# Performance work log

Hardware: AMD Instinct MI355X
Metric: run time of the kernel (lower is better)

Reference implementation:

```python
import jax, jax.numpy as jnp
import numpy as np

N_VOXELS = 400000
GRID = 128
KSIZE = 3
GROUPS = 4
C_IN = 64
C_OUT = 64


def _build_rulebook(n, grid, ksize, seed=0):
    """Build submanifold-conv neighbor map on host with numpy.

    Returns coords-free neighbor_idx [n, ksize**3] int32; entry k is the index of
    the active voxel at offset k from voxel i, or -1 if that site is inactive.
    """
    rng = np.random.default_rng(seed)
    lin = rng.choice(grid ** 3, size=n, replace=False).astype(np.int64)
    x = lin // (grid * grid)
    y = (lin // grid) % grid
    z = lin % grid
    order = np.argsort(lin)
    sorted_keys = lin[order]
    r = ksize // 2
    nb = np.full((n, ksize ** 3), -1, dtype=np.int32)
    k = 0
    for dx in range(-r, r + 1):
        for dy in range(-r, r + 1):
            for dz in range(-r, r + 1):
                nx, ny, nz = x + dx, y + dy, z + dz
                inb = (nx >= 0) & (nx < grid) & (ny >= 0) & (ny < grid) & (nz >= 0) & (nz < grid)
                nkey = nx * grid * grid + ny * grid + nz
                pos = np.searchsorted(sorted_keys, nkey)
                pos_c = np.minimum(pos, n - 1)
                found = inb & (sorted_keys[pos_c] == nkey)
                nb[:, k] = np.where(found, order[pos_c], -1).astype(np.int32)
                k += 1
    return nb


def setup_inputs() -> dict:
    key = jax.random.key(0)
    k1, k2, k3 = jax.random.split(key, 3)
    cpg_in = C_IN // GROUPS
    cpg_out = C_OUT // GROUPS
    features = jax.random.normal(k1, (N_VOXELS, C_IN), dtype=jnp.float32)
    # weight[g, k, ci, co] for each group g and kernel offset k
    weight = jax.random.normal(k2, (GROUPS, KSIZE ** 3, cpg_in, cpg_out), dtype=jnp.float32) * (1.0 / np.sqrt(cpg_in * KSIZE ** 3))
    bias = jax.random.normal(k3, (C_OUT,), dtype=jnp.float32) * 0.01
    neighbor_idx = jnp.asarray(_build_rulebook(N_VOXELS, GRID, KSIZE))
    return {"features": features, "weight": weight, "bias": bias, "neighbor_idx": neighbor_idx}


def reference(features, weight, bias, neighbor_idx):
    # Grouped submanifold sparse conv: gather -> grouped matmul -> accumulate,
    # over the fixed set of K^3 kernel offsets (output sites == input sites).
    N = features.shape[0]
    G, K, cin, cout = weight.shape
    feat = features.reshape(N, G, cin)
    mask = neighbor_idx >= 0                      # [N, K]
    idx = jnp.where(mask, neighbor_idx, 0)        # safe gather index
    out = jnp.zeros((N, G, cout), dtype=features.dtype)
    for k in range(K):  # K=27 fixed small loop over kernel offsets
        gath = feat[idx[:, k]] * mask[:, k, None, None].astype(features.dtype)  # [N, G, cin]
        out = out + jnp.einsum('ngc,gcd->ngd', gath, weight[:, k])
    out = out.reshape(N, G * cout) + bias
    return out
```

## Files before the change

kernel.cpp:

```cpp
#include <hip/hip_runtime.h>
#include <hip/hip_fp16.h>

#define NVOX 400000
#define KVOL 27
#define CTOT 64
#define NTILES (NVOX / 16)
#define NPAIR 14
#define WFRAG_HALVES (4 * NPAIR * 64 * 8)

#define FEATH_OFF 0
#define WFRAG_OFF 51200000

typedef __attribute__((ext_vector_type(8))) _Float16 half8;
typedef __attribute__((ext_vector_type(4))) float float4v;

__global__ void cvt_feat_kernel(const float* __restrict__ f, _Float16* __restrict__ fh) {
    int t = blockIdx.x * blockDim.x + threadIdx.x;
    const int total = NVOX * CTOT / 8;
    if (t >= total) return;
    const float4* fp = (const float4*)f + (size_t)t * 2;
    float4 a = fp[0], b = fp[1];
    union { _Float16 h[8]; uint4 u; } r;
    r.h[0] = (_Float16)a.x; r.h[1] = (_Float16)a.y;
    r.h[2] = (_Float16)a.z; r.h[3] = (_Float16)a.w;
    r.h[4] = (_Float16)b.x; r.h[5] = (_Float16)b.y;
    r.h[6] = (_Float16)b.z; r.h[7] = (_Float16)b.w;
    ((uint4*)fh)[t] = r.u;
}

__global__ void cvt_w_kernel(const float* __restrict__ w, _Float16* __restrict__ wf) {
    int t = blockIdx.x * blockDim.x + threadIdx.x;
    if (t >= WFRAG_HALVES) return;
    int j = t & 7;
    int l = (t >> 3) & 63;
    int gp = t >> 9;
    int p = gp % NPAIR;
    int g = gp / NPAIR;
    int co = l & 15;
    int quad = l >> 4;
    int ko = 2 * p + (quad >> 1);
    int ci = (quad & 1) * 8 + j;
    float val = (ko < KVOL) ? w[((g * KVOL + ko) * 16 + ci) * 16 + co] : 0.f;
    wf[t] = (_Float16)val;
}

__global__ __launch_bounds__(256) void conv_main_kernel(
        const _Float16* __restrict__ fh,
        const uint4*    __restrict__ wfrag,
        const float*    __restrict__ bias,
        const int*      __restrict__ nb,
        float* __restrict__ out) {
    __shared__ int s_nb[16 * 28];
    const int tile = blockIdx.x;
    const int t = threadIdx.x;

    const int* src = nb + (size_t)tile * (16 * KVOL);
    for (int j = t; j < 16 * KVOL; j += 256) {
        int v = j / KVOL;
        int k = j - v * KVOL;
        s_nb[v * 28 + k] = src[j];
    }
    if (t < 16) s_nb[t * 28 + 27] = -1;

    const int lane = t & 63;
    const int g = t >> 6;
    const int v = lane & 15;
    const int quad = lane >> 4;
    const int q2 = quad >> 1;
    const int half = quad & 1;

    uint4 wB[NPAIR];
#pragma unroll
    for (int p = 0; p < NPAIR; ++p)
        wB[p] = wfrag[(g * NPAIR + p) * 64 + lane];

    __syncthreads();

    int idx[NPAIR];
#pragma unroll
    for (int p = 0; p < NPAIR; ++p)
        idx[p] = s_nb[v * 28 + 2 * p + q2];

    const _Float16* fbase = fh + g * 16 + half * 8;
    const _Float16* zp = (const _Float16*)wfrag + 6912;

    uint4 a[NPAIR];
#pragma unroll
    for (int p = 0; p < NPAIR; ++p) {
        const _Float16* rp = (idx[p] >= 0) ? (fbase + (size_t)idx[p] * CTOT) : zp;
        a[p] = *(const uint4*)rp;
    }
    __builtin_amdgcn_sched_barrier(0);

    float4v acc0 = {0.f, 0.f, 0.f, 0.f};
    float4v acc1 = {0.f, 0.f, 0.f, 0.f};
#pragma unroll
    for (int p = 0; p < NPAIR; p += 2) {
        acc0 = __builtin_amdgcn_mfma_f32_16x16x32_f16(
            __builtin_bit_cast(half8, a[p]),
            __builtin_bit_cast(half8, wB[p]), acc0, 0, 0, 0);
        acc1 = __builtin_amdgcn_mfma_f32_16x16x32_f16(
            __builtin_bit_cast(half8, a[p + 1]),
            __builtin_bit_cast(half8, wB[p + 1]), acc1, 0, 0, 0);
    }

    const int co = lane & 15;
    const float breg = bias[g * 16 + co];
    float* ob = out + ((size_t)(tile * 16 + quad * 4)) * CTOT + g * 16 + co;
#pragma unroll
    for (int r = 0; r < 4; ++r)
        ob[(size_t)r * CTOT] = acc0[r] + acc1[r] + breg;
}

extern "C" void kernel_launch(void* const* d_in, const int* in_sizes, int n_in,
                              void* d_out, int out_size, void* d_ws, size_t ws_size,
                              hipStream_t stream) {
    const float* features = (const float*)d_in[0];
    const float* weight   = (const float*)d_in[1];
    const float* bias     = (const float*)d_in[2];
    const int*   nb       = (const int*)d_in[3];
    float* out = (float*)d_out;

    char* ws = (char*)d_ws;
    _Float16* featH = (_Float16*)(ws + FEATH_OFF);
    _Float16* wf    = (_Float16*)(ws + WFRAG_OFF);

    cvt_feat_kernel<<<(NVOX * CTOT / 8 + 255) / 256, 256, 0, stream>>>(features, featH);
    cvt_w_kernel<<<(WFRAG_HALVES + 255) / 256, 256, 0, stream>>>(weight, wf);
    conv_main_kernel<<<NTILES, 256, 0, stream>>>(featH, (const uint4*)wf, bias, nb, out);
}
```

Before: 330.4 us.

## Process multiple tiles per block with double-buffered neighbor staging and XCD remap

Each workgroup now handles 10 consecutive 16-voxel tiles, so weight fragments are loaded once per block rather than once per tile. The neighbor-index staging is double-buffered in shared memory, and the gather for the next tile is issued before the MFMAs of the current one to overlap memory latency with compute. Block IDs are remapped so that contiguous tile ranges land on the same XCD for cache locality, and inactive neighbors are zeroed with a predicate instead of a load from a zero pointer. This raises register pressure through two fragment arrays, and there is one barrier per tile.

```diff
diff --git a/kernel.cpp b/kernel.cpp
--- a/kernel.cpp
+++ b/kernel.cpp
@@ -6,6 +6,8 @@
 #define CTOT 64
 #define NTILES (NVOX / 16)
 #define NPAIR 14
+#define TPB 10
+#define NBLOCKS (NTILES / TPB)
 #define WFRAG_HALVES (4 * NPAIR * 64 * 8)
 
 #define FEATH_OFF 0
@@ -44,72 +46,102 @@
     wf[t] = (_Float16)val;
 }
 
-__global__ __launch_bounds__(256) void conv_main_kernel(
+__global__ __launch_bounds__(256, 2) void conv_main_kernel(
         const _Float16* __restrict__ fh,
         const uint4*    __restrict__ wfrag,
         const float*    __restrict__ bias,
         const int*      __restrict__ nb,
         float* __restrict__ out) {
-    __shared__ int s_nb[16 * 28];
-    const int tile = blockIdx.x;
+    __shared__ int s_nb[2][16 * KVOL];
     const int t = threadIdx.x;
-
-    const int* src = nb + (size_t)tile * (16 * KVOL);
-    for (int j = t; j < 16 * KVOL; j += 256) {
-        int v = j / KVOL;
-        int k = j - v * KVOL;
-        s_nb[v * 28 + k] = src[j];
-    }
-    if (t < 16) s_nb[t * 28 + 27] = -1;
-
     const int lane = t & 63;
     const int g = t >> 6;
     const int v = lane & 15;
     const int quad = lane >> 4;
     const int q2 = quad >> 1;
     const int half = quad & 1;
+    const int co = lane & 15;
+
+    {
+    }
+    const int q_ = NBLOCKS / 8, r_ = NBLOCKS % 8;
+    const int xcd = blockIdx.x % 8;
+    const int chunk = blockIdx.x / 8;
+    const int wgid = (xcd < r_ ? xcd * (q_ + 1) : r_ * (q_ + 1) + (xcd - r_) * q_) + chunk;
+    const int tile0 = wgid * TPB;
 
     uint4 wB[NPAIR];
 #pragma unroll
     for (int p = 0; p < NPAIR; ++p)
         wB[p] = wfrag[(g * NPAIR + p) * 64 + lane];
 
-    __syncthreads();
+    const _Float16* fbase = fh + g * 16 + half * 8;
+    const float breg = bias[g * 16 + co];
+    const int vb = v * KVOL;
 
-    int idx[NPAIR];
-#pragma unroll
-    for (int p = 0; p < NPAIR; ++p)
-        idx[p] = s_nb[v * 28 + 2 * p + q2];
-
-    const _Float16* fbase = fh + g * 16 + half * 8;
-    const _Float16* zp = (const _Float16*)wfrag + 6912;
-
-    uint4 a[NPAIR];
-#pragma unroll
-    for (int p = 0; p < NPAIR; ++p) {
-        const _Float16* rp = (idx[p] >= 0) ? (fbase + (size_t)idx[p] * CTOT) : zp;
-        a[p] = *(const uint4*)rp;
-    }
-    __builtin_amdgcn_sched_barrier(0);
-
-    float4v acc0 = {0.f, 0.f, 0.f, 0.f};
-    float4v acc1 = {0.f, 0.f, 0.f, 0.f};
-#pragma unroll
-    for (int p = 0; p < NPAIR; p += 2) {
-        acc0 = __builtin_amdgcn_mfma_f32_16x16x32_f16(
-            __builtin_bit_cast(half8, a[p]),
-            __builtin_bit_cast(half8, wB[p]), acc0, 0, 0, 0);
-        acc1 = __builtin_amdgcn_mfma_f32_16x16x32_f16(
-            __builtin_bit_cast(half8, a[p + 1]),
-            __builtin_bit_cast(half8, wB[p + 1]), acc1, 0, 0, 0);
+#define STAGE(b, tile)                                              \
+    {                                                               \
+        const int* src = nb + (size_t)(tile) * (16 * KVOL);         \
+        for (int j = t; j < 16 * KVOL; j += 256)                    \
+            s_nb[(b)][j] = src[j];                                  \
     }
 
-    const int co = lane & 15;
-    const float breg = bias[g * 16 + co];
-    float* ob = out + ((size_t)(tile * 16 + quad * 4)) * CTOT + g * 16 + co;
+#define GATHER(dst, b)                                              \
+    {                                                               \
+        int ix[NPAIR];                                              \
+        _Pragma("unroll")                                           \
+        for (int p = 0; p < NPAIR - 1; ++p)                         \
+            ix[p] = s_nb[(b)][vb + 2 * p + q2];                     \
+        ix[NPAIR - 1] = (q2 == 0) ? s_nb[(b)][vb + 26] : -1;        \
+        _Pragma("unroll")                                           \
+        for (int p = 0; p < NPAIR; ++p) {                           \
+            uint4 z = {0u, 0u, 0u, 0u};                             \
+            dst[p] = z;                                             \
+            if (ix[p] >= 0)                                         \
+                dst[p] = *(const uint4*)(fbase + (size_t)ix[p] * CTOT); \
+        }                                                           \
+    }
+
+    STAGE(0, tile0);
+    __syncthreads();
+    uint4 aA[NPAIR];
+    GATHER(aA, 0);
+
 #pragma unroll
-    for (int r = 0; r < 4; ++r)
-        ob[(size_t)r * CTOT] = acc0[r] + acc1[r] + breg;
+    for (int tt = 0; tt < TPB; ++tt) {
+        uint4 aB[NPAIR];
+        if (tt + 1 < TPB) {
+            STAGE((tt + 1) & 1, tile0 + tt + 1);
+            __syncthreads();
+            GATHER(aB, (tt + 1) & 1);
+        }
+        __builtin_amdgcn_sched_barrier(0);
+
+        float4v acc0 = {0.f, 0.f, 0.f, 0.f};
+        float4v acc1 = {0.f, 0.f, 0.f, 0.f};
+#pragma unroll
+        for (int p = 0; p < NPAIR; p += 2) {
+            acc0 = __builtin_amdgcn_mfma_f32_16x16x32_f16(
+                __builtin_bit_cast(half8, aA[p]),
+                __builtin_bit_cast(half8, wB[p]), acc0, 0, 0, 0);
+            acc1 = __builtin_amdgcn_mfma_f32_16x16x32_f16(
+                __builtin_bit_cast(half8, aA[p + 1]),
+                __builtin_bit_cast(half8, wB[p + 1]), acc1, 0, 0, 0);
+        }
+
+        float* ob = out + ((size_t)((tile0 + tt) * 16 + quad * 4)) * CTOT + g * 16 + co;
+#pragma unroll
+        for (int r = 0; r < 4; ++r)
+            ob[(size_t)r * CTOT] = acc0[r] + acc1[r] + breg;
+
+        if (tt + 1 < TPB) {
+#pragma unroll
+            for (int p = 0; p < NPAIR; ++p)
+                aA[p] = aB[p];
+        }
+    }
+#undef STAGE
+#undef GATHER
 }
 
 extern "C" void kernel_launch(void* const* d_in, const int* in_sizes, int n_in,
@@ -127,5 +159,5 @@
 
     cvt_feat_kernel<<<(NVOX * CTOT / 8 + 255) / 256, 256, 0, stream>>>(features, featH);
     cvt_w_kernel<<<(WFRAG_HALVES + 255) / 256, 256, 0, stream>>>(weight, wf);
-    conv_main_kernel<<<NTILES, 256, 0, stream>>>(featH, (const uint4*)wf, bias, nb, out);
+    conv_main_kernel<<<NBLOCKS, 256, 0, stream>>>(featH, (const uint4*)wf, bias, nb, out);
 }
```

Result: faster. 319.9 us (-3.2%).
